# Kernel optimization log

Hardware: AMD Instinct MI355X
Metric: run time of the kernel (lower is better)

The kernel has to match this reference:

```python
import jax, jax.numpy as jnp
import numpy as np

BN_EPS = 1e-5


def setup_inputs() -> dict:
    key = jax.random.key(0)
    ks = jax.random.split(key, 10)
    B, C, H, W = 8, 512, 64, 64      # batch, in_channels, spatial
    K, V, O = 256, 256, 512          # key_channels, value_channels, out_channels
    s = 0.02
    return {
        "x": jax.random.normal(ks[0], (B, C, H, W), jnp.float32),
        # 1x1 convs are channel matmuls: weight [out_c, in_c]
        "wv": jax.random.normal(ks[1], (V, C), jnp.float32) * s,
        "bv": jax.random.normal(ks[2], (V,), jnp.float32) * s,
        "wk": jax.random.normal(ks[3], (K, C), jnp.float32) * s,
        "bk": jax.random.normal(ks[4], (K,), jnp.float32) * s,
        # BatchNorm2d (inference mode: running stats)
        "gamma": jnp.ones((K,), jnp.float32),
        "beta": jnp.zeros((K,), jnp.float32),
        "rmean": jax.random.normal(ks[5], (K,), jnp.float32) * 0.1,
        "rvar": jax.random.uniform(ks[6], (K,), jnp.float32, 0.5, 1.5),
        # output 1x1 conv W (zero-init in torch; use small random for a useful baseline)
        "wW": jax.random.normal(ks[7], (O, V), jnp.float32) * s,
        "bW": jax.random.normal(ks[8], (O,), jnp.float32) * s,
    }


def reference(x, wv, bv, wk, bk, gamma, beta, rmean, rvar, wW, bW):
    B, C, H, W = x.shape
    N = H * W
    xf = x.reshape(B, C, N)                                   # [B, C, N]

    # f_value: 1x1 conv -> [B, V, N]
    value = jnp.einsum('vc,bcn->bvn', wv, xf) + bv[:, None]

    # f_key (= f_query, shared module): conv1x1 + BN(inference) + ReLU -> [B, K, N]
    k = jnp.einsum('kc,bcn->bkn', wk, xf) + bk[:, None]
    scale = gamma / jnp.sqrt(rvar + BN_EPS)
    k = (k - rmean[:, None]) * scale[:, None] + beta[:, None]
    k = jax.nn.relu(k)

    # sim_map = query^T @ key * K^-0.5; query == key since f_query is f_key
    Kc = k.shape[1]
    sim = jnp.einsum('bkn,bkm->bnm', k, k) * (Kc ** -0.5)     # [B, N, N]
    sim = jax.nn.softmax(sim, axis=-1)

    # context = sim @ value^T -> [B, V, N]
    ctx = jnp.einsum('bnm,bvm->bvn', sim, value)

    # output 1x1 conv W
    out = jnp.einsum('ov,bvn->bon', wW, ctx) + bW[:, None]    # [B, O, N]
    return out.reshape(B, -1, H, W)
```

## Files before the change

kernel.cpp:

```cpp
#include <hip/hip_runtime.h>
#include <hip/hip_bf16.h>
#include <stdint.h>


typedef __bf16 bf16;
typedef bf16 bf16x4 __attribute__((ext_vector_type(4)));
typedef bf16 bf16x8 __attribute__((ext_vector_type(8)));
typedef float f32x4 __attribute__((ext_vector_type(4)));
typedef float f32x16 __attribute__((ext_vector_type(16)));

#define Bb 8
#define Cc 512
#define Nn 4096
#define Kc 256
#define Vv 256
#define Oo 512
#define BN_EPS 1e-5f
#define QSCALE 0.300280601f

static __device__ __forceinline__ f32x16 mfma32(bf16x8 a, bf16x8 b, f32x16 c) {
    return __builtin_amdgcn_mfma_f32_32x32x16_bf16(a, b, c, 0, 0, 0);
}
static __device__ __forceinline__ unsigned cvtpk(float lo, float hi) {
    unsigned r;
    asm("v_cvt_pk_bf16_f32 %0, %1, %2" : "=v"(r) : "v"(lo), "v"(hi));
    return r;
}
#define GLD16(gp, lp) __builtin_amdgcn_global_load_lds( \
    (const __attribute__((address_space(1))) unsigned int*)(gp), \
    (__attribute__((address_space(3))) unsigned int*)(lp), 16, 0, 0)

__global__ __launch_bounds__(256) void prep_kernel(
        const float* __restrict__ wk, const float* __restrict__ wv,
        const float* __restrict__ wW, const float* __restrict__ bk,
        const float* __restrict__ gamma, const float* __restrict__ beta,
        const float* __restrict__ rmean, const float* __restrict__ rvar,
        bf16* __restrict__ wkv, bf16* __restrict__ wWb, float* __restrict__ shift2) {
    int idx = blockIdx.x * 256 + threadIdx.x;
    if (idx < 131072) {
        int kc = idx >> 9;
        float sc = gamma[kc] * rsqrtf(rvar[kc] + BN_EPS);
        wkv[idx] = (bf16)(wk[idx] * sc);
    } else if (idx < 262144) {
        wkv[idx] = (bf16)(wv[idx - 131072]);
    } else if (idx < 393216) {
        int j = idx - 262144;
        wWb[j] = (bf16)(wW[j]);
    } else if (idx < 393472) {
        int kc = idx - 393216;
        float sc = gamma[kc] * rsqrtf(rvar[kc] + BN_EPS);
        shift2[kc] = (bk[kc] - rmean[kc]) * sc + beta[kc];
    }
}

__global__ __launch_bounds__(256) void transpose_kernel(
        const float* __restrict__ x, bf16* __restrict__ xT) {
    int b = blockIdx.z, c0 = blockIdx.y * 32, n0 = blockIdx.x * 64;
    __shared__ float lds[32][65];
    int t = threadIdx.x;
    int r = t >> 3, s = t & 7;
    const float* src = x + ((size_t)(b * Cc + c0 + r)) * Nn + n0 + s * 8;
    float4 v0 = *(const float4*)src;
    float4 v1 = *(const float4*)(src + 4);
    lds[r][s * 8 + 0] = v0.x; lds[r][s * 8 + 1] = v0.y;
    lds[r][s * 8 + 2] = v0.z; lds[r][s * 8 + 3] = v0.w;
    lds[r][s * 8 + 4] = v1.x; lds[r][s * 8 + 5] = v1.y;
    lds[r][s * 8 + 6] = v1.z; lds[r][s * 8 + 7] = v1.w;
    __syncthreads();
    int wr = t >> 2, part = t & 3;
    bf16x8 o;
#pragma unroll
    for (int j = 0; j < 8; ++j) o[j] = (bf16)lds[part * 8 + j][wr];
    *(bf16x8*)(xT + ((size_t)(b * Nn + n0 + wr)) * Cc + c0 + part * 8) = o;
}

__global__ __launch_bounds__(256, 2) void proj_kernel(
        const bf16* __restrict__ xT, const bf16* __restrict__ wkv,
        const float* __restrict__ shift2, const float* __restrict__ bv,
        bf16* __restrict__ kT, bf16* __restrict__ val) {
    int tile = blockIdx.x;
    int b = tile >> 6, n0 = (tile & 63) * 64;
    int t = threadIdx.x, w = t >> 6, l = t & 63, li = l & 31, hi = l >> 5;
    int nsub = w & 1, ochalf = w >> 1;
    int n = n0 + nsub * 32 + li;

    const bf16* xrow = xT + ((size_t)(b * Nn + n)) * Cc + hi * 8;
    bf16x8 bfr[32];
#pragma unroll
    for (int cs = 0; cs < 32; ++cs) bfr[cs] = *(const bf16x8*)(xrow + cs * 16);

    f32x16 Z;
#pragma unroll
    for (int r = 0; r < 16; ++r) Z[r] = 0.f;

    for (int ocb = 0; ocb < 8; ++ocb) {
        int ocbase = ochalf * 256 + ocb * 32;
        const bf16* arow = wkv + (size_t)(ocbase + li) * Cc + hi * 8;
        f32x16 acc = mfma32(*(const bf16x8*)(arow), bfr[0], Z);
#pragma unroll
        for (int cs = 1; cs < 32; ++cs)
            acc = mfma32(*(const bf16x8*)(arow + cs * 16), bfr[cs], acc);
        if (ocbase < 256) {
#pragma unroll
            for (int rq = 0; rq < 4; ++rq) {
                int kc0 = ocbase + rq * 8 + hi * 4;
                bf16x4 o;
#pragma unroll
                for (int r = 0; r < 4; ++r) {
                    float v = acc[rq * 4 + r] + shift2[kc0 + r];
                    o[r] = (bf16)(fmaxf(v, 0.f) * QSCALE);
                }
                *(bf16x4*)(kT + ((size_t)(b * Nn + n)) * Kc + kc0) = o;
            }
        } else {
#pragma unroll
            for (int rq = 0; rq < 4; ++rq)
#pragma unroll
                for (int r = 0; r < 4; ++r) {
                    int vc = ocbase - 256 + rq * 8 + hi * 4 + r;
                    val[((size_t)(b * Vv + vc)) * Nn + n] = (bf16)(acc[rq * 4 + r] + bv[vc]);
                }
        }
    }
}

__global__ __launch_bounds__(256, 2) void flash_kernel(
        const bf16* __restrict__ kT, const bf16* __restrict__ val,
        bf16* __restrict__ ctxP, float* __restrict__ ml) {
    __shared__ __align__(16) char lds[65536];
    const int t = threadIdx.x;
    const int b = blockIdx.x;
    const int s = blockIdx.z;
    const int w = t >> 6, l = t & 63, li = l & 31, hi = l >> 5;
    const int n = blockIdx.y * 128 + w * 32 + li;
    const int m0 = s * (Nn / 2);
    const int NT = (Nn / 2) / 32;

    const bf16* kTb  = kT  + (size_t)b * Nn * Kc;
    const bf16* valb = val + (size_t)b * Vv * Nn;

    const bf16* qrow = kTb + (size_t)n * Kc;
    bf16x8 qf[16];
#pragma unroll
    for (int cs = 0; cs < 16; ++cs) qf[cs] = *(const bf16x8*)(qrow + cs * 16 + hi * 8);

    int koff[4];
#pragma unroll
    for (int j = 0; j < 4; ++j) {
        int r = j * 8 + (t >> 5);
        koff[j] = r * Kc + ((t & 31) ^ r) * 8;
    }
    char* kdst = lds + w * 1024;
    char* vdst = lds + 16384 + w * 1024;

    const int kq = li * 512 + ((li ^ hi) << 4);
    const int pv = hi * 4096 + li * 16;

    f32x16 Z;
#pragma unroll
    for (int r = 0; r < 16; ++r) Z[r] = 0.f;
    f32x16 ctx[8];
#pragma unroll
    for (int vc = 0; vc < 8; ++vc) ctx[vc] = Z;
    float M = -1.0e30f, L = 0.f;

    auto STAGE = [&](int tile, int bb) {
        const bf16* kg = kTb + (size_t)(m0 + tile * 32) * Kc;
        const bf16* vg = valb + (size_t)t * Nn + (m0 + tile * 32);
#pragma unroll
        for (int j = 0; j < 4; ++j) GLD16(kg + koff[j], kdst + bb * 32768 + j * 4096);
#pragma unroll
        for (int j = 0; j < 4; ++j) GLD16(vg + j * 8, vdst + bb * 32768 + j * 4096);
    };

    STAGE(0, 0);
    for (int it = 0; it < NT; ++it) {
        const int bb = it & 1;
        if (it + 1 < NT) {
            STAGE(it + 1, bb ^ 1);
            asm volatile("s_waitcnt vmcnt(8)" ::: "memory");
        } else {
            asm volatile("s_waitcnt vmcnt(0)" ::: "memory");
        }
        __builtin_amdgcn_s_barrier();
        __builtin_amdgcn_sched_barrier(0);
        const char* kb = lds + bb * 32768;
        const char* vb = kb + 16384;

        __builtin_amdgcn_s_setprio(1);
        f32x16 S = mfma32(*(const bf16x8*)(kb + kq), qf[0], Z);
#pragma unroll
        for (int cs = 1; cs < 16; ++cs) {
            bf16x8 a0 = *(const bf16x8*)(kb + (kq ^ (cs << 5)));
            S = mfma32(a0, qf[cs], S);
        }
        __builtin_amdgcn_s_setprio(0);

        float m0a = fmaxf(fmaxf(S[0], S[1]), fmaxf(S[2], S[3]));
        float m0b = fmaxf(fmaxf(S[4], S[5]), fmaxf(S[6], S[7]));
        float m0c = fmaxf(fmaxf(S[8], S[9]), fmaxf(S[10], S[11]));
        float m0d = fmaxf(fmaxf(S[12], S[13]), fmaxf(S[14], S[15]));
        float tmax = fmaxf(fmaxf(m0a, m0b), fmaxf(m0c, m0d));
        tmax = fmaxf(tmax, __shfl_xor(tmax, 32, 64));
        if (__any(tmax > M + 8.f)) {
            float newM = fmaxf(M, tmax);
            float alpha = exp2f(M - newM);
            M = newM;
            L *= alpha;
#pragma unroll
            for (int vc = 0; vc < 8; ++vc) ctx[vc] = ctx[vc] * alpha;
        }
#pragma unroll
        for (int r = 0; r < 16; ++r) S[r] = exp2f(S[r] - M);
        float t0 = (S[0] + S[1]) + (S[2] + S[3]);
        float t1 = (S[4] + S[5]) + (S[6] + S[7]);
        float t2 = (S[8] + S[9]) + (S[10] + S[11]);
        float t3 = (S[12] + S[13]) + (S[14] + S[15]);
        float tsum = (t0 + t1) + (t2 + t3);
        tsum += __shfl_xor(tsum, 32, 64);
        L += tsum;

        unsigned c0 = cvtpk(S[0], S[1]),  c1 = cvtpk(S[2], S[3]);
        unsigned c2 = cvtpk(S[4], S[5]),  c3 = cvtpk(S[6], S[7]);
        unsigned c4 = cvtpk(S[8], S[9]),  c5 = cvtpk(S[10], S[11]);
        unsigned c6 = cvtpk(S[12], S[13]), c7 = cvtpk(S[14], S[15]);
        auto r0 = __builtin_amdgcn_permlane32_swap(c0, c2, false, false);
        auto r1 = __builtin_amdgcn_permlane32_swap(c1, c3, false, false);
        auto r2 = __builtin_amdgcn_permlane32_swap(c4, c6, false, false);
        auto r3 = __builtin_amdgcn_permlane32_swap(c5, c7, false, false);
        union U8 { unsigned u[4]; bf16x8 v; } B1, B2;
        B1.u[0] = r0[0]; B1.u[1] = r1[0]; B1.u[2] = r0[1]; B1.u[3] = r1[1];
        B2.u[0] = r2[0]; B2.u[1] = r3[0]; B2.u[2] = r2[1]; B2.u[3] = r3[1];

        __builtin_amdgcn_s_setprio(1);
#pragma unroll
        for (int vc = 0; vc < 8; ++vc) {
            bf16x8 va = *(const bf16x8*)(vb + pv + vc * 512);
            ctx[vc] = mfma32(va, B1.v, ctx[vc]);
        }
#pragma unroll
        for (int vc = 0; vc < 8; ++vc) {
            bf16x8 va = *(const bf16x8*)(vb + pv + 8192 + vc * 512);
            ctx[vc] = mfma32(va, B2.v, ctx[vc]);
        }
        __builtin_amdgcn_s_setprio(0);
        if (it + 1 < NT) {
            __builtin_amdgcn_sched_barrier(0);
            __builtin_amdgcn_s_barrier();
        }
    }

    size_t idx = (size_t)(s * Bb + b) * Nn + n;
    bf16* crow = ctxP + idx * Vv;
#pragma unroll
    for (int vc = 0; vc < 8; ++vc) {
#pragma unroll
        for (int rq = 0; rq < 4; ++rq) {
            bf16x4 o;
#pragma unroll
            for (int r = 0; r < 4; ++r) o[r] = (bf16)ctx[vc][rq * 4 + r];
            *(bf16x4*)(crow + vc * 32 + rq * 8 + hi * 4) = o;
        }
    }
    if (hi == 0) {
        float2 v; v.x = M; v.y = L;
        *(float2*)(ml + idx * 2) = v;
    }
}

__global__ __launch_bounds__(256, 2) void out_kernel(
        const bf16* __restrict__ ctxP, const float* __restrict__ ml,
        const bf16* __restrict__ wWb, const float* __restrict__ bW,
        float* __restrict__ out) {
    int tile = blockIdx.x;
    int b = tile >> 6, n0 = (tile & 63) * 64;
    int t = threadIdx.x, w = t >> 6, l = t & 63, li = l & 31, hi = l >> 5;
    int nsub = w & 1, ochalf = w >> 1;
    int n = n0 + nsub * 32 + li;

    size_t iA = (size_t)b * Nn + n;
    size_t iB = (size_t)(Bb + b) * Nn + n;
    const bf16* ca = ctxP + iA * Vv + hi * 8;
    const bf16* cb = ctxP + iB * Vv + hi * 8;
    float MA = ml[iA * 2], LA = ml[iA * 2 + 1];
    float MB = ml[iB * 2], LB = ml[iB * 2 + 1];
    float Mx = fmaxf(MA, MB);
    float wA = exp2f(MA - Mx), wB = exp2f(MB - Mx);
    float inv = 1.f / (LA * wA + LB * wB);
    float sA = wA * inv, sB = wB * inv;

    bf16x8 bfr[16];
#pragma unroll
    for (int cs = 0; cs < 16; ++cs) {
        bf16x8 fa = *(const bf16x8*)(ca + cs * 16);
        bf16x8 fb = *(const bf16x8*)(cb + cs * 16);
        bf16x8 o;
#pragma unroll
        for (int j = 0; j < 8; ++j)
            o[j] = (bf16)(sA * (float)fa[j] + sB * (float)fb[j]);
        bfr[cs] = o;
    }

    f32x16 Z;
#pragma unroll
    for (int r = 0; r < 16; ++r) Z[r] = 0.f;

    for (int ocb = 0; ocb < 8; ++ocb) {
        int ocbase = ochalf * 256 + ocb * 32;
        const bf16* arow = wWb + (size_t)(ocbase + li) * Vv + hi * 8;
        f32x16 acc = mfma32(*(const bf16x8*)(arow), bfr[0], Z);
#pragma unroll
        for (int cs = 1; cs < 16; ++cs)
            acc = mfma32(*(const bf16x8*)(arow + cs * 16), bfr[cs], acc);
#pragma unroll
        for (int rq = 0; rq < 4; ++rq)
#pragma unroll
            for (int r = 0; r < 4; ++r) {
                int oc = ocbase + rq * 8 + hi * 4 + r;
                out[((size_t)(b * Oo + oc)) * Nn + n] = acc[rq * 4 + r] + bW[oc];
            }
    }
}

extern "C" void kernel_launch(void* const* d_in, const int* in_sizes, int n_in,
                              void* d_out, int out_size, void* d_ws, size_t ws_size,
                              hipStream_t stream) {
    const float* x     = (const float*)d_in[0];
    const float* wv    = (const float*)d_in[1];
    const float* bv    = (const float*)d_in[2];
    const float* wk    = (const float*)d_in[3];
    const float* bk    = (const float*)d_in[4];
    const float* gamma = (const float*)d_in[5];
    const float* beta  = (const float*)d_in[6];
    const float* rmean = (const float*)d_in[7];
    const float* rvar  = (const float*)d_in[8];
    const float* wW    = (const float*)d_in[9];
    const float* bW    = (const float*)d_in[10];
    float* out = (float*)d_out;

    char* ws = (char*)d_ws;
    bf16*  xT     = (bf16*)(ws + 0);
    bf16*  ctxP   = (bf16*)(ws + 0);
    bf16*  kTp    = (bf16*)(ws + 33554432);
    bf16*  valp   = (bf16*)(ws + 50331648);
    bf16*  wkv    = (bf16*)(ws + 67108864);
    bf16*  wWb    = (bf16*)(ws + 67633152);
    float* shift2 = (float*)(ws + 67895296);
    float* ml     = (float*)(ws + 68157440);

    prep_kernel<<<dim3(1537), dim3(256), 0, stream>>>(wk, wv, wW, bk, gamma, beta,
                                                      rmean, rvar, wkv, wWb, shift2);
    transpose_kernel<<<dim3(64, 16, 8), dim3(256), 0, stream>>>(x, xT);
    proj_kernel<<<dim3(512), dim3(256), 0, stream>>>(xT, wkv, shift2, bv, kTp, valp);
    flash_kernel<<<dim3(8, 32, 2), dim3(256), 0, stream>>>(kTp, valp, ctxP, ml);
    out_kernel<<<dim3(512), dim3(256), 0, stream>>>(ctxP, ml, wWb, bW, out);
}
```

Measured before the change: 292.8 us.

## Software-pipeline flash loop: overlap previous PV MFMAs with current QK, split K/V staging

Restructures the flash attention loop so the P·V MFMAs for the previous tile run right after the QK^T MFMAs of the current tile, with separate K and V double buffers and a second barrier before the V prefetch. The QK chain is split into two independent accumulators, and the projection and output GEMM kernels compute two 32-row output blocks per pass. This targets MFMA dependency stalls and the gap between the softmax and the PV phase. The cost is more registers (carried B fragments, two accumulators), an extra barrier per iteration and a separate final PV step after the loop.

```diff
diff --git a/kernel.cpp b/kernel.cpp
--- a/kernel.cpp
+++ b/kernel.cpp
@@ -93,13 +93,7 @@
 #pragma unroll
     for (int r = 0; r < 16; ++r) Z[r] = 0.f;
 
-    for (int ocb = 0; ocb < 8; ++ocb) {
-        int ocbase = ochalf * 256 + ocb * 32;
-        const bf16* arow = wkv + (size_t)(ocbase + li) * Cc + hi * 8;
-        f32x16 acc = mfma32(*(const bf16x8*)(arow), bfr[0], Z);
-#pragma unroll
-        for (int cs = 1; cs < 32; ++cs)
-            acc = mfma32(*(const bf16x8*)(arow + cs * 16), bfr[cs], acc);
+    auto writeout = [&](const f32x16& acc, int ocbase) {
         if (ocbase < 256) {
 #pragma unroll
             for (int rq = 0; rq < 4; ++rq) {
@@ -121,6 +115,21 @@
                     val[((size_t)(b * Vv + vc)) * Nn + n] = (bf16)(acc[rq * 4 + r] + bv[vc]);
                 }
         }
+    };
+
+    for (int ocp = 0; ocp < 4; ++ocp) {
+        int base0 = ochalf * 256 + ocp * 64;
+        const bf16* a0 = wkv + (size_t)(base0 + li) * Cc + hi * 8;
+        const bf16* a1 = a0 + (size_t)32 * Cc;
+        f32x16 acc0 = mfma32(*(const bf16x8*)(a0), bfr[0], Z);
+        f32x16 acc1 = mfma32(*(const bf16x8*)(a1), bfr[0], Z);
+#pragma unroll
+        for (int cs = 1; cs < 32; ++cs) {
+            acc0 = mfma32(*(const bf16x8*)(a0 + cs * 16), bfr[cs], acc0);
+            acc1 = mfma32(*(const bf16x8*)(a1 + cs * 16), bfr[cs], acc1);
+        }
+        writeout(acc0, base0);
+        writeout(acc1, base0 + 32);
     }
 }
 
@@ -151,7 +160,7 @@
         koff[j] = r * Kc + ((t & 31) ^ r) * 8;
     }
     char* kdst = lds + w * 1024;
-    char* vdst = lds + 16384 + w * 1024;
+    char* vdst = lds + 32768 + w * 1024;
 
     const int kq = li * 512 + ((li ^ hi) << 4);
     const int pv = hi * 4096 + li * 16;
@@ -164,37 +173,63 @@
     for (int vc = 0; vc < 8; ++vc) ctx[vc] = Z;
     float M = -1.0e30f, L = 0.f;
 
-    auto STAGE = [&](int tile, int bb) {
+    union U8 { unsigned u[4]; bf16x8 v; };
+    U8 B1p, B2p;
+#pragma unroll
+    for (int j = 0; j < 4; ++j) { B1p.u[j] = 0u; B2p.u[j] = 0u; }
+
+    auto STAGEK = [&](int tile, int bb2) {
         const bf16* kg = kTb + (size_t)(m0 + tile * 32) * Kc;
+#pragma unroll
+        for (int j = 0; j < 4; ++j) GLD16(kg + koff[j], kdst + bb2 * 16384 + j * 4096);
+    };
+    auto STAGEV = [&](int tile, int bb2) {
         const bf16* vg = valb + (size_t)t * Nn + (m0 + tile * 32);
 #pragma unroll
-        for (int j = 0; j < 4; ++j) GLD16(kg + koff[j], kdst + bb * 32768 + j * 4096);
-#pragma unroll
-        for (int j = 0; j < 4; ++j) GLD16(vg + j * 8, vdst + bb * 32768 + j * 4096);
+        for (int j = 0; j < 4; ++j) GLD16(vg + j * 8, vdst + bb2 * 16384 + j * 4096);
     };
 
-    STAGE(0, 0);
+    STAGEK(0, 0);
+    STAGEV(0, 0);
     for (int it = 0; it < NT; ++it) {
         const int bb = it & 1;
         if (it + 1 < NT) {
-            STAGE(it + 1, bb ^ 1);
+            STAGEK(it + 1, bb ^ 1);
             asm volatile("s_waitcnt vmcnt(8)" ::: "memory");
         } else {
-            asm volatile("s_waitcnt vmcnt(0)" ::: "memory");
-        }
+            asm volatile("s_waitcnt vmcnt(4)" ::: "memory");
+        }
+        __builtin_amdgcn_sched_barrier(0);
         __builtin_amdgcn_s_barrier();
         __builtin_amdgcn_sched_barrier(0);
-        const char* kb = lds + bb * 32768;
-        const char* vb = kb + 16384;
+        const char* kb = lds + bb * 16384;
+        const char* vprev = it ? lds + 32768 + (bb ^ 1) * 16384 : lds;
 
         __builtin_amdgcn_s_setprio(1);
-        f32x16 S = mfma32(*(const bf16x8*)(kb + kq), qf[0], Z);
-#pragma unroll
-        for (int cs = 1; cs < 16; ++cs) {
-            bf16x8 a0 = *(const bf16x8*)(kb + (kq ^ (cs << 5)));
-            S = mfma32(a0, qf[cs], S);
+        f32x16 Sa = mfma32(*(const bf16x8*)(kb + kq), qf[0], Z);
+        f32x16 Sb = mfma32(*(const bf16x8*)(kb + (kq ^ 32)), qf[1], Z);
+#pragma unroll
+        for (int cs = 2; cs < 16; cs += 2) {
+            Sa = mfma32(*(const bf16x8*)(kb + (kq ^ (cs << 5))), qf[cs], Sa);
+            Sb = mfma32(*(const bf16x8*)(kb + (kq ^ ((cs + 1) << 5))), qf[cs + 1], Sb);
+        }
+#pragma unroll
+        for (int vc = 0; vc < 8; ++vc) {
+            bf16x8 va = *(const bf16x8*)(vprev + pv + vc * 512);
+            ctx[vc] = mfma32(va, B1p.v, ctx[vc]);
+        }
+#pragma unroll
+        for (int vc = 0; vc < 8; ++vc) {
+            bf16x8 va = *(const bf16x8*)(vprev + pv + 8192 + vc * 512);
+            ctx[vc] = mfma32(va, B2p.v, ctx[vc]);
         }
         __builtin_amdgcn_s_setprio(0);
+        f32x16 S = Sa + Sb;
+
+        __builtin_amdgcn_sched_barrier(0);
+        __builtin_amdgcn_s_barrier();
+        __builtin_amdgcn_sched_barrier(0);
+        if (it + 1 < NT) STAGEV(it + 1, bb ^ 1);
 
         float m0a = fmaxf(fmaxf(S[0], S[1]), fmaxf(S[2], S[3]));
         float m0b = fmaxf(fmaxf(S[4], S[5]), fmaxf(S[6], S[7]));
@@ -228,26 +263,24 @@
         auto r1 = __builtin_amdgcn_permlane32_swap(c1, c3, false, false);
         auto r2 = __builtin_amdgcn_permlane32_swap(c4, c6, false, false);
         auto r3 = __builtin_amdgcn_permlane32_swap(c5, c7, false, false);
-        union U8 { unsigned u[4]; bf16x8 v; } B1, B2;
-        B1.u[0] = r0[0]; B1.u[1] = r1[0]; B1.u[2] = r0[1]; B1.u[3] = r1[1];
-        B2.u[0] = r2[0]; B2.u[1] = r3[0]; B2.u[2] = r2[1]; B2.u[3] = r3[1];
-
-        __builtin_amdgcn_s_setprio(1);
-#pragma unroll
-        for (int vc = 0; vc < 8; ++vc) {
-            bf16x8 va = *(const bf16x8*)(vb + pv + vc * 512);
-            ctx[vc] = mfma32(va, B1.v, ctx[vc]);
-        }
-#pragma unroll
-        for (int vc = 0; vc < 8; ++vc) {
-            bf16x8 va = *(const bf16x8*)(vb + pv + 8192 + vc * 512);
-            ctx[vc] = mfma32(va, B2.v, ctx[vc]);
-        }
-        __builtin_amdgcn_s_setprio(0);
-        if (it + 1 < NT) {
-            __builtin_amdgcn_sched_barrier(0);
-            __builtin_amdgcn_s_barrier();
-        }
+        B1p.u[0] = r0[0]; B1p.u[1] = r1[0]; B1p.u[2] = r0[1]; B1p.u[3] = r1[1];
+        B2p.u[0] = r2[0]; B2p.u[1] = r3[0]; B2p.u[2] = r2[1]; B2p.u[3] = r3[1];
+    }
+
+    asm volatile("s_waitcnt vmcnt(0)" ::: "memory");
+    __builtin_amdgcn_sched_barrier(0);
+    __builtin_amdgcn_s_barrier();
+    __builtin_amdgcn_sched_barrier(0);
+    const char* vlast = lds + 32768 + ((NT - 1) & 1) * 16384;
+#pragma unroll
+    for (int vc = 0; vc < 8; ++vc) {
+        bf16x8 va = *(const bf16x8*)(vlast + pv + vc * 512);
+        ctx[vc] = mfma32(va, B1p.v, ctx[vc]);
+    }
+#pragma unroll
+    for (int vc = 0; vc < 8; ++vc) {
+        bf16x8 va = *(const bf16x8*)(vlast + pv + 8192 + vc * 512);
+        ctx[vc] = mfma32(va, B2p.v, ctx[vc]);
     }
 
     size_t idx = (size_t)(s * Bb + b) * Nn + n;
@@ -305,19 +338,25 @@
 #pragma unroll
     for (int r = 0; r < 16; ++r) Z[r] = 0.f;
 
-    for (int ocb = 0; ocb < 8; ++ocb) {
-        int ocbase = ochalf * 256 + ocb * 32;
-        const bf16* arow = wWb + (size_t)(ocbase + li) * Vv + hi * 8;
-        f32x16 acc = mfma32(*(const bf16x8*)(arow), bfr[0], Z);
-#pragma unroll
-        for (int cs = 1; cs < 16; ++cs)
-            acc = mfma32(*(const bf16x8*)(arow + cs * 16), bfr[cs], acc);
+    for (int ocp = 0; ocp < 4; ++ocp) {
+        int base0 = ochalf * 256 + ocp * 64;
+        const bf16* a0 = wWb + (size_t)(base0 + li) * Vv + hi * 8;
+        const bf16* a1 = a0 + (size_t)32 * Vv;
+        f32x16 acc0 = mfma32(*(const bf16x8*)(a0), bfr[0], Z);
+        f32x16 acc1 = mfma32(*(const bf16x8*)(a1), bfr[0], Z);
+#pragma unroll
+        for (int cs = 1; cs < 16; ++cs) {
+            acc0 = mfma32(*(const bf16x8*)(a0 + cs * 16), bfr[cs], acc0);
+            acc1 = mfma32(*(const bf16x8*)(a1 + cs * 16), bfr[cs], acc1);
+        }
 #pragma unroll
         for (int rq = 0; rq < 4; ++rq)
 #pragma unroll
             for (int r = 0; r < 4; ++r) {
-                int oc = ocbase + rq * 8 + hi * 4 + r;
-                out[((size_t)(b * Oo + oc)) * Nn + n] = acc[rq * 4 + r] + bW[oc];
+                int oc0 = base0 + rq * 8 + hi * 4 + r;
+                out[((size_t)(b * Oo + oc0)) * Nn + n] = acc0[rq * 4 + r] + bW[oc0];
+                int oc1 = oc0 + 32;
+                out[((size_t)(b * Oo + oc1)) * Nn + n] = acc1[rq * 4 + r] + bW[oc1];
             }
     }
 }
```

Measured after the change: 317.5 us. 8.4% more time.

## Fuse x transpose into projection kernel and pair MFMA accumulators

Applied to the files above, without the earlier changes.

Removes the separate transpose kernel and its bf16 xT round trip through global memory. The projection kernel now loads fp32 x tiles directly, transposes them through LDS, and builds its bf16 B fragments in registers. Both the projection and output kernels now run two independent 32-row MFMA accumulator chains per loop iteration, which adds instruction-level parallelism. The cost is 16 LDS-synchronized load phases per block and higher register pressure from the second accumulator.

```diff
diff --git a/kernel.cpp b/kernel.cpp
--- a/kernel.cpp
+++ b/kernel.cpp
@@ -53,29 +53,8 @@
     }
 }
 
-__global__ __launch_bounds__(256) void transpose_kernel(
-        const float* __restrict__ x, bf16* __restrict__ xT) {
-    int b = blockIdx.z, c0 = blockIdx.y * 32, n0 = blockIdx.x * 64;
-    __shared__ float lds[32][65];
-    int t = threadIdx.x;
-    int r = t >> 3, s = t & 7;
-    const float* src = x + ((size_t)(b * Cc + c0 + r)) * Nn + n0 + s * 8;
-    float4 v0 = *(const float4*)src;
-    float4 v1 = *(const float4*)(src + 4);
-    lds[r][s * 8 + 0] = v0.x; lds[r][s * 8 + 1] = v0.y;
-    lds[r][s * 8 + 2] = v0.z; lds[r][s * 8 + 3] = v0.w;
-    lds[r][s * 8 + 4] = v1.x; lds[r][s * 8 + 5] = v1.y;
-    lds[r][s * 8 + 6] = v1.z; lds[r][s * 8 + 7] = v1.w;
-    __syncthreads();
-    int wr = t >> 2, part = t & 3;
-    bf16x8 o;
-#pragma unroll
-    for (int j = 0; j < 8; ++j) o[j] = (bf16)lds[part * 8 + j][wr];
-    *(bf16x8*)(xT + ((size_t)(b * Nn + n0 + wr)) * Cc + c0 + part * 8) = o;
-}
-
 __global__ __launch_bounds__(256, 2) void proj_kernel(
-        const bf16* __restrict__ xT, const bf16* __restrict__ wkv,
+        const float* __restrict__ x, const bf16* __restrict__ wkv,
         const float* __restrict__ shift2, const float* __restrict__ bv,
         bf16* __restrict__ kT, bf16* __restrict__ val) {
     int tile = blockIdx.x;
@@ -83,32 +62,46 @@
     int t = threadIdx.x, w = t >> 6, l = t & 63, li = l & 31, hi = l >> 5;
     int nsub = w & 1, ochalf = w >> 1;
     int n = n0 + nsub * 32 + li;
-
-    const bf16* xrow = xT + ((size_t)(b * Nn + n)) * Cc + hi * 8;
+    int ncol = nsub * 32 + li;
+
+    __shared__ float xs[32][65];
     bf16x8 bfr[32];
-#pragma unroll
-    for (int cs = 0; cs < 32; ++cs) bfr[cs] = *(const bf16x8*)(xrow + cs * 16);
+    int r = t >> 3, sseg = t & 7;
+#pragma unroll
+    for (int p = 0; p < 16; ++p) {
+        const float* src = x + ((size_t)(b * Cc + p * 32 + r)) * Nn + n0 + sseg * 8;
+        float4 v0 = *(const float4*)src;
+        float4 v1 = *(const float4*)(src + 4);
+        if (p) __syncthreads();
+        xs[r][sseg * 8 + 0] = v0.x; xs[r][sseg * 8 + 1] = v0.y;
+        xs[r][sseg * 8 + 2] = v0.z; xs[r][sseg * 8 + 3] = v0.w;
+        xs[r][sseg * 8 + 4] = v1.x; xs[r][sseg * 8 + 5] = v1.y;
+        xs[r][sseg * 8 + 6] = v1.z; xs[r][sseg * 8 + 7] = v1.w;
+        __syncthreads();
+        bf16x8 e0, e1;
+#pragma unroll
+        for (int j = 0; j < 8; ++j) {
+            e0[j] = (bf16)xs[hi * 8 + j][ncol];
+            e1[j] = (bf16)xs[16 + hi * 8 + j][ncol];
+        }
+        bfr[2 * p] = e0;
+        bfr[2 * p + 1] = e1;
+    }
 
     f32x16 Z;
 #pragma unroll
-    for (int r = 0; r < 16; ++r) Z[r] = 0.f;
-
-    for (int ocb = 0; ocb < 8; ++ocb) {
-        int ocbase = ochalf * 256 + ocb * 32;
-        const bf16* arow = wkv + (size_t)(ocbase + li) * Cc + hi * 8;
-        f32x16 acc = mfma32(*(const bf16x8*)(arow), bfr[0], Z);
-#pragma unroll
-        for (int cs = 1; cs < 32; ++cs)
-            acc = mfma32(*(const bf16x8*)(arow + cs * 16), bfr[cs], acc);
+    for (int rr = 0; rr < 16; ++rr) Z[rr] = 0.f;
+
+    auto writeout = [&](const f32x16& acc, int ocbase) {
         if (ocbase < 256) {
 #pragma unroll
             for (int rq = 0; rq < 4; ++rq) {
                 int kc0 = ocbase + rq * 8 + hi * 4;
                 bf16x4 o;
 #pragma unroll
-                for (int r = 0; r < 4; ++r) {
-                    float v = acc[rq * 4 + r] + shift2[kc0 + r];
-                    o[r] = (bf16)(fmaxf(v, 0.f) * QSCALE);
+                for (int rr = 0; rr < 4; ++rr) {
+                    float v = acc[rq * 4 + rr] + shift2[kc0 + rr];
+                    o[rr] = (bf16)(fmaxf(v, 0.f) * QSCALE);
                 }
                 *(bf16x4*)(kT + ((size_t)(b * Nn + n)) * Kc + kc0) = o;
             }
@@ -116,11 +109,26 @@
 #pragma unroll
             for (int rq = 0; rq < 4; ++rq)
 #pragma unroll
-                for (int r = 0; r < 4; ++r) {
-                    int vc = ocbase - 256 + rq * 8 + hi * 4 + r;
-                    val[((size_t)(b * Vv + vc)) * Nn + n] = (bf16)(acc[rq * 4 + r] + bv[vc]);
+                for (int rr = 0; rr < 4; ++rr) {
+                    int vc = ocbase - 256 + rq * 8 + hi * 4 + rr;
+                    val[((size_t)(b * Vv + vc)) * Nn + n] = (bf16)(acc[rq * 4 + rr] + bv[vc]);
                 }
         }
+    };
+
+    for (int ocp = 0; ocp < 4; ++ocp) {
+        int base0 = ochalf * 256 + ocp * 64;
+        const bf16* a0 = wkv + (size_t)(base0 + li) * Cc + hi * 8;
+        const bf16* a1 = a0 + (size_t)32 * Cc;
+        f32x16 acc0 = mfma32(*(const bf16x8*)(a0), bfr[0], Z);
+        f32x16 acc1 = mfma32(*(const bf16x8*)(a1), bfr[0], Z);
+#pragma unroll
+        for (int cs = 1; cs < 32; ++cs) {
+            acc0 = mfma32(*(const bf16x8*)(a0 + cs * 16), bfr[cs], acc0);
+            acc1 = mfma32(*(const bf16x8*)(a1 + cs * 16), bfr[cs], acc1);
+        }
+        writeout(acc0, base0);
+        writeout(acc1, base0 + 32);
     }
 }
 
@@ -305,19 +313,25 @@
 #pragma unroll
     for (int r = 0; r < 16; ++r) Z[r] = 0.f;
 
-    for (int ocb = 0; ocb < 8; ++ocb) {
-        int ocbase = ochalf * 256 + ocb * 32;
-        const bf16* arow = wWb + (size_t)(ocbase + li) * Vv + hi * 8;
-        f32x16 acc = mfma32(*(const bf16x8*)(arow), bfr[0], Z);
-#pragma unroll
-        for (int cs = 1; cs < 16; ++cs)
-            acc = mfma32(*(const bf16x8*)(arow + cs * 16), bfr[cs], acc);
+    for (int ocp = 0; ocp < 4; ++ocp) {
+        int base0 = ochalf * 256 + ocp * 64;
+        const bf16* a0 = wWb + (size_t)(base0 + li) * Vv + hi * 8;
+        const bf16* a1 = a0 + (size_t)32 * Vv;
+        f32x16 acc0 = mfma32(*(const bf16x8*)(a0), bfr[0], Z);
+        f32x16 acc1 = mfma32(*(const bf16x8*)(a1), bfr[0], Z);
+#pragma unroll
+        for (int cs = 1; cs < 16; ++cs) {
+            acc0 = mfma32(*(const bf16x8*)(a0 + cs * 16), bfr[cs], acc0);
+            acc1 = mfma32(*(const bf16x8*)(a1 + cs * 16), bfr[cs], acc1);
+        }
 #pragma unroll
         for (int rq = 0; rq < 4; ++rq)
 #pragma unroll
             for (int r = 0; r < 4; ++r) {
-                int oc = ocbase + rq * 8 + hi * 4 + r;
-                out[((size_t)(b * Oo + oc)) * Nn + n] = acc[rq * 4 + r] + bW[oc];
+                int oc0 = base0 + rq * 8 + hi * 4 + r;
+                out[((size_t)(b * Oo + oc0)) * Nn + n] = acc0[rq * 4 + r] + bW[oc0];
+                int oc1 = oc0 + 32;
+                out[((size_t)(b * Oo + oc1)) * Nn + n] = acc1[rq * 4 + r] + bW[oc1];
             }
     }
 }
@@ -339,7 +353,6 @@
     float* out = (float*)d_out;
 
     char* ws = (char*)d_ws;
-    bf16*  xT     = (bf16*)(ws + 0);
     bf16*  ctxP   = (bf16*)(ws + 0);
     bf16*  kTp    = (bf16*)(ws + 33554432);
     bf16*  valp   = (bf16*)(ws + 50331648);
@@ -350,8 +363,7 @@
 
     prep_kernel<<<dim3(1537), dim3(256), 0, stream>>>(wk, wv, wW, bk, gamma, beta,
                                                       rmean, rvar, wkv, wWb, shift2);
-    transpose_kernel<<<dim3(64, 16, 8), dim3(256), 0, stream>>>(x, xT);
-    proj_kernel<<<dim3(512), dim3(256), 0, stream>>>(xT, wkv, shift2, bv, kTp, valp);
+    proj_kernel<<<dim3(512), dim3(256), 0, stream>>>(x, wkv, shift2, bv, kTp, valp);
     flash_kernel<<<dim3(8, 32, 2), dim3(256), 0, stream>>>(kTp, valp, ctxP, ml);
     out_kernel<<<dim3(512), dim3(256), 0, stream>>>(ctxP, ml, wWb, bW, out);
 }
```

Result: faster. 279.3 us (-4.6%).
